# Optimization experiments

Measured on AMD Instinct MI355X. Metric: run time of the kernel, lower is better.

The kernel has to match this reference:

```python
import jax, jax.numpy as jnp
import numpy as np

N = 50000   # nodes
E = 800000  # edges
H = 128     # hidden_dim
H2 = H // 2


def setup_inputs() -> dict:
    key = jax.random.key(0)
    ks = jax.random.split(key, 12)
    s = 0.05  # weight scale for numerical sanity
    d = {}
    d['coord_x'] = jax.random.normal(ks[0], (N,), jnp.float32)
    d['coord_y'] = jax.random.normal(ks[1], (N,), jnp.float32)
    d['W1'] = jax.random.normal(ks[2], (3, H), jnp.float32) * s
    d['b1'] = jnp.zeros((H,), jnp.float32)
    d['W2'] = jax.random.normal(ks[3], (H, H), jnp.float32) * s
    d['b2'] = jnp.zeros((H,), jnp.float32)
    d['W3'] = jax.random.normal(ks[4], (H, H), jnp.float32) * s
    d['b3'] = jnp.zeros((H,), jnp.float32)
    d['W4'] = jax.random.normal(ks[5], (H, H), jnp.float32) * s
    d['b4'] = jnp.zeros((H,), jnp.float32)
    d['W5'] = jax.random.normal(ks[6], (H, H), jnp.float32) * s
    d['b5'] = jnp.zeros((H,), jnp.float32)
    d['Wl1'] = jax.random.normal(ks[7], (H, H2), jnp.float32) * s
    d['bl1'] = jnp.zeros((H2,), jnp.float32)
    d['Wl2'] = jax.random.normal(ks[8], (H2, 1), jnp.float32) * s
    d['bl2'] = jnp.zeros((1,), jnp.float32)
    d['src'] = jax.random.randint(ks[9], (E,), 0, N, dtype=jnp.int32)
    d['dst'] = jax.random.randint(ks[10], (E,), 0, N, dtype=jnp.int32)
    return d


def reference(coord_x, coord_y, W1, b1, W2, b2, W3, b3, W4, b4, W5, b5,
              Wl1, bl1, Wl2, bl2, src, dst):
    ones_e = jnp.ones((E,), jnp.float32)
    in_deg = jax.ops.segment_sum(ones_e, dst, num_segments=N)   # [N]
    out_deg = jax.ops.segment_sum(ones_e, src, num_segments=N)  # [N]
    # DGL GraphConv norm='both': D_out^{-1/2} on src side, D_in^{-1/2} on dst side,
    # degrees clamped to min 1.
    norm_s = (jnp.maximum(out_deg, 1.0) ** -0.5)[:, None]  # [N,1]
    norm_d = (jnp.maximum(in_deg, 1.0) ** -0.5)[:, None]   # [N,1]

    def gconv(h, W, b):
        msg = (h * norm_s)[src]                                   # [E,F] gather
        agg = jax.ops.segment_sum(msg, dst, num_segments=N)       # [N,F] scatter-add
        return (agg * norm_d) @ W + b

    # node features: [in_degree, x, y]
    h = jnp.stack([in_deg, coord_x, coord_y], axis=1)  # [N,3]
    for W, b in ((W1, b1), (W2, b2), (W3, b3), (W4, b4), (W5, b5)):
        h = jax.nn.relu(gconv(h, W, b))

    graph_emb = jnp.mean(h, axis=0, keepdims=True)          # [1,H] mean_nodes
    h_emb = jax.nn.relu(graph_emb @ Wl1 + bl1)              # dropout p=0 -> identity
    pred = jax.nn.sigmoid(h_emb @ Wl2 + bl2)                # [1,1]
    return pred, graph_emb, h
```

## Files before the change

### kernel.cpp

```cpp
#include <hip/hip_runtime.h>
#include <hip/hip_bf16.h>
#include <math.h>

#define NN 50000
#define NE 800000
#define HD 128
#define NB 196
#define CAP 5120
#define B1_EPB 1024

typedef __attribute__((ext_vector_type(8))) short bf16x8v;
typedef __attribute__((ext_vector_type(4))) float f32x4v;

static __device__ __forceinline__ unsigned short f2bf(float x) {
    union { float f; unsigned u; } v; v.f = x;
    unsigned r = v.u + 0x7fff + ((v.u >> 16) & 1);
    return (unsigned short)(r >> 16);
}

__global__ __launch_bounds__(256) void bucket_kernel(const int* __restrict__ src,
                                                     const int* __restrict__ dst,
                                                     int* __restrict__ dcur,
                                                     int* __restrict__ scur,
                                                     ushort2* __restrict__ dbucket,
                                                     unsigned short* __restrict__ sbucket) {
    __shared__ int hd[NB], hsb[NB], cd[NB], cs[NB];
    int t = threadIdx.x;
    if (t < NB) { hd[t] = 0; hsb[t] = 0; }
    __syncthreads();
    int d[4], s[4];
    int e0 = blockIdx.x * B1_EPB + t;
    #pragma unroll
    for (int j = 0; j < 4; ++j) {
        int e = e0 + j * 256;
        if (e < NE) {
            d[j] = dst[e]; s[j] = src[e];
            atomicAdd(&hd[d[j] >> 8], 1);
            atomicAdd(&hsb[s[j] >> 8], 1);
        } else d[j] = -1;
    }
    __syncthreads();
    if (t < NB) {
        cd[t] = atomicAdd(&dcur[t], hd[t]);
        cs[t] = atomicAdd(&scur[t], hsb[t]);
    }
    __syncthreads();
    #pragma unroll
    for (int j = 0; j < 4; ++j) {
        if (d[j] >= 0) {
            int b = d[j] >> 8;
            int p = atomicAdd(&cd[b], 1);
            if (p < CAP) dbucket[(long)b * CAP + p] = make_ushort2((unsigned short)d[j],
                                                                   (unsigned short)s[j]);
            int bs = s[j] >> 8;
            int p2 = atomicAdd(&cs[bs], 1);
            if (p2 < CAP) sbucket[(long)bs * CAP + p2] = (unsigned short)s[j];
        }
    }
}

__global__ __launch_bounds__(256) void csr_out_kernel(const ushort2* __restrict__ dbucket,
                                                      const int* __restrict__ dcur,
                                                      const unsigned short* __restrict__ sbucket,
                                                      const int* __restrict__ scur,
                                                      int* __restrict__ row_ptr,
                                                      unsigned short* __restrict__ col,
                                                      int* __restrict__ out_cnt) {
    __shared__ int buf[256];
    __shared__ int hist[256];
    __shared__ int cur[256];
    int k = blockIdx.x, t = threadIdx.x;

    int tot = (t < NB) ? min(dcur[t], CAP) : 0;
    buf[t] = tot;
    __syncthreads();
    for (int o = 1; o < 256; o <<= 1) {
        int a = (t >= o) ? buf[t - o] : 0;
        __syncthreads();
        buf[t] += a;
        __syncthreads();
    }
    int base = (k > 0) ? buf[k - 1] : 0;
    int cnt = min(dcur[k], CAP);

    hist[t] = 0;
    __syncthreads();
    const ushort2* bk = dbucket + (long)k * CAP;
    for (int e = t; e < cnt; e += 256) atomicAdd(&hist[bk[e].x & 255], 1);
    __syncthreads();
    int h = hist[t];

    buf[t] = h;
    __syncthreads();
    for (int o = 1; o < 256; o <<= 1) {
        int a = (t >= o) ? buf[t - o] : 0;
        __syncthreads();
        buf[t] += a;
        __syncthreads();
    }
    int start = base + buf[t] - h;
    int id = (k << 8) + t;
    if (id < NN) row_ptr[id] = start;
    if (k == NB - 1 && t == 0) row_ptr[NN] = base + cnt;
    cur[t] = start;
    __syncthreads();

    for (int e = t; e < cnt; e += 256) {
        ushort2 p = bk[e];
        int pos = atomicAdd(&cur[p.x & 255], 1);
        col[pos] = p.y;
    }

    __syncthreads();
    hist[t] = 0;
    __syncthreads();
    int scnt = min(scur[k], CAP);
    const unsigned short* sk = sbucket + (long)k * CAP;
    for (int e = t; e < scnt; e += 256) atomicAdd(&hist[sk[e] & 255], 1);
    __syncthreads();
    if (id < NN) out_cnt[id] = hist[t];
}

__global__ __launch_bounds__(256) void initw_kernel(const float* __restrict__ cx,
                                                    const float* __restrict__ cy,
                                                    const int* __restrict__ row_ptr,
                                                    const int* __restrict__ out_cnt,
                                                    const float* __restrict__ W2,
                                                    const float* __restrict__ W3,
                                                    const float* __restrict__ W4,
                                                    const float* __restrict__ W5,
                                                    float* __restrict__ norm_s,
                                                    float* __restrict__ norm_d,
                                                    float* __restrict__ h0s,
                                                    unsigned short* __restrict__ Wt,
                                                    float* __restrict__ embsum) {
    int bid = blockIdx.x, t = threadIdx.x;
    if (bid < NB) {
        int i = (bid << 8) + t;
        if (i < NN) {
            float id = (float)(row_ptr[i + 1] - row_ptr[i]);
            float od = (float)out_cnt[i];
            float ns = 1.0f / sqrtf(fmaxf(od, 1.0f));
            norm_s[i] = ns;
            norm_d[i] = 1.0f / sqrtf(fmaxf(id, 1.0f));
            h0s[i * 3 + 0] = id * ns;
            h0s[i * 3 + 1] = cx[i] * ns;
            h0s[i * 3 + 2] = cy[i] * ns;
        }
    } else {
        int gid = ((bid - NB) << 8) + t;
        int l = gid >> 14, idx = gid & 16383;
        int n = idx >> 7, k = idx & 127;
        const float* W = (l == 0) ? W2 : (l == 1) ? W3 : (l == 2) ? W4 : W5;
        Wt[gid] = f2bf(W[k * 128 + n]);
        if (bid == NB && t < 128) embsum[t] = 0.0f;
    }
}

__global__ __launch_bounds__(256) void layer1_kernel(const int* __restrict__ row_ptr,
                                                     const unsigned short* __restrict__ col,
                                                     const float* __restrict__ h0s,
                                                     const float* __restrict__ norm_d,
                                                     const float* __restrict__ norm_s,
                                                     const float* __restrict__ W1,
                                                     const float* __restrict__ b1,
                                                     unsigned short* __restrict__ h1s) {
    __shared__ float la3[256][3];
    __shared__ float lw[3][128];
    __shared__ float lb[128];
    int t = threadIdx.x;
    int n0 = blockIdx.x << 8;
    if (t < 128) {
        lw[0][t] = W1[t]; lw[1][t] = W1[128 + t]; lw[2][t] = W1[256 + t];
        lb[t] = b1[t];
    }
    int n = n0 + t;
    if (n < NN) {
        float a0 = 0.f, a1 = 0.f, a2 = 0.f;
        int end = row_ptr[n + 1];
        for (int e = row_ptr[n]; e < end; ++e) {
            int s = col[e];
            a0 += h0s[s * 3 + 0];
            a1 += h0s[s * 3 + 1];
            a2 += h0s[s * 3 + 2];
        }
        float nd = norm_d[n];
        la3[t][0] = a0 * nd; la3[t][1] = a1 * nd; la3[t][2] = a2 * nd;
    }
    __syncthreads();
    #pragma unroll 4
    for (int i = 0; i < 128; ++i) {
        int idx = (i << 8) + t;
        int r = idx >> 7, c = idx & 127;
        int nn = n0 + r;
        if (nn < NN) {
            float v = la3[r][0] * lw[0][c] + la3[r][1] * lw[1][c]
                    + la3[r][2] * lw[2][c] + lb[c];
            h1s[((long)nn << 7) + c] = f2bf(fmaxf(v, 0.f) * norm_s[nn]);
        }
    }
}

__global__ __launch_bounds__(256) void fused_layer16_kernel(const int* __restrict__ row_ptr,
                                                            const unsigned short* __restrict__ col,
                                                            const unsigned int* __restrict__ hin,
                                                            const float* __restrict__ norm_d,
                                                            const float* __restrict__ norm_s,
                                                            const unsigned short* __restrict__ Wt,
                                                            const float* __restrict__ bias,
                                                            unsigned short* __restrict__ hout,
                                                            float* __restrict__ out_f32,
                                                            float* __restrict__ embsum) {
    __shared__ unsigned int lA[16][68];
    __shared__ float ldscol[4][128];
    int t = threadIdx.x;
    int wv = t >> 6, lane = t & 63;
    int m0 = blockIdx.x << 4;

    const unsigned int* hb = hin + lane;
    #pragma unroll
    for (int half = 0; half < 2; ++half) {
        int rA = (half << 3) + wv;
        int rB = rA + 4;
        int nA = m0 + rA, nB = m0 + rB;
        int eA = row_ptr[nA], endA = row_ptr[nA + 1];
        int eB = row_ptr[nB], endB = row_ptr[nB + 1];
        float axA = 0.f, ayA = 0.f, axB = 0.f, ayB = 0.f;

        while (eA + 3 < endA && eB + 3 < endB) {
            unsigned uA[4], uB[4];
            #pragma unroll
            for (int j = 0; j < 4; ++j) uA[j] = hb[(long)col[eA + j] << 6];
            #pragma unroll
            for (int j = 0; j < 4; ++j) uB[j] = hb[(long)col[eB + j] << 6];
            #pragma unroll
            for (int j = 0; j < 4; ++j) {
                axA += __uint_as_float(uA[j] << 16);
                ayA += __uint_as_float(uA[j] & 0xffff0000u);
                axB += __uint_as_float(uB[j] << 16);
                ayB += __uint_as_float(uB[j] & 0xffff0000u);
            }
            eA += 4; eB += 4;
        }
        for (; eA + 3 < endA; eA += 4) {
            unsigned u[4];
            #pragma unroll
            for (int j = 0; j < 4; ++j) u[j] = hb[(long)col[eA + j] << 6];
            #pragma unroll
            for (int j = 0; j < 4; ++j) {
                axA += __uint_as_float(u[j] << 16);
                ayA += __uint_as_float(u[j] & 0xffff0000u);
            }
        }
        for (; eA < endA; ++eA) {
            unsigned u0 = hb[(long)col[eA] << 6];
            axA += __uint_as_float(u0 << 16);
            ayA += __uint_as_float(u0 & 0xffff0000u);
        }
        for (; eB + 3 < endB; eB += 4) {
            unsigned u[4];
            #pragma unroll
            for (int j = 0; j < 4; ++j) u[j] = hb[(long)col[eB + j] << 6];
            #pragma unroll
            for (int j = 0; j < 4; ++j) {
                axB += __uint_as_float(u[j] << 16);
                ayB += __uint_as_float(u[j] & 0xffff0000u);
            }
        }
        for (; eB < endB; ++eB) {
            unsigned u0 = hb[(long)col[eB] << 6];
            axB += __uint_as_float(u0 << 16);
            ayB += __uint_as_float(u0 & 0xffff0000u);
        }

        float ndA = norm_d[nA], ndB = norm_d[nB];
        lA[rA][lane] = (unsigned)f2bf(axA * ndA) | ((unsigned)f2bf(ayA * ndA) << 16);
        lA[rB][lane] = (unsigned)f2bf(axB * ndB) | ((unsigned)f2bf(ayB * ndB) << 16);
    }
    __syncthreads();

    int fr = lane & 15, kq = lane >> 4;
    bf16x8v a0 = *(const bf16x8v*)&lA[fr][ 0 + (kq << 2)];
    bf16x8v a1 = *(const bf16x8v*)&lA[fr][16 + (kq << 2)];
    bf16x8v a2 = *(const bf16x8v*)&lA[fr][32 + (kq << 2)];
    bf16x8v a3 = *(const bf16x8v*)&lA[fr][48 + (kq << 2)];

    float4 scv = make_float4(1.f, 1.f, 1.f, 1.f);
    if (!out_f32) scv = *(const float4*)(norm_s + m0 + (kq << 2));

    #pragma unroll
    for (int j = 0; j < 2; ++j) {
        int n0 = ((wv << 1) + j) << 4;
        const unsigned short* wb = Wt + ((n0 + fr) << 7) + (kq << 3);
        f32x4v acc = {0.f, 0.f, 0.f, 0.f};
        acc = __builtin_amdgcn_mfma_f32_16x16x32_bf16(a0, *(const bf16x8v*)(wb + 0),  acc, 0, 0, 0);
        acc = __builtin_amdgcn_mfma_f32_16x16x32_bf16(a1, *(const bf16x8v*)(wb + 32), acc, 0, 0, 0);
        acc = __builtin_amdgcn_mfma_f32_16x16x32_bf16(a2, *(const bf16x8v*)(wb + 64), acc, 0, 0, 0);
        acc = __builtin_amdgcn_mfma_f32_16x16x32_bf16(a3, *(const bf16x8v*)(wb + 96), acc, 0, 0, 0);

        int c = n0 + fr;
        float bv = bias[c];
        if (out_f32) {
            float cs = 0.f;
            #pragma unroll
            for (int r = 0; r < 4; ++r) {
                int mr = m0 + (kq << 2) + r;
                float v = fmaxf(acc[r] + bv, 0.f);
                out_f32[((long)mr << 7) + c] = v;
                cs += v;
            }
            ldscol[kq][c] = cs;
        } else {
            #pragma unroll
            for (int r = 0; r < 4; ++r) {
                int mr = m0 + (kq << 2) + r;
                float v = fmaxf(acc[r] + bv, 0.f);
                float sc = (r == 0) ? scv.x : (r == 1) ? scv.y : (r == 2) ? scv.z : scv.w;
                hout[((long)mr << 7) + c] = f2bf(v * sc);
            }
        }
    }

    if (out_f32) {
        __syncthreads();
        if (t < 128) {
            float s = ldscol[0][t] + ldscol[1][t] + ldscol[2][t] + ldscol[3][t];
            atomicAdd(&embsum[t], s);
        }
    }
}

__global__ __launch_bounds__(128) void head_kernel(const float* __restrict__ embsum,
                                                   const float* __restrict__ Wl1,
                                                   const float* __restrict__ bl1,
                                                   const float* __restrict__ Wl2,
                                                   const float* __restrict__ bl2,
                                                   float* __restrict__ d_out) {
    __shared__ float emb[128];
    __shared__ float hemb[64];
    int t = threadIdx.x;
    float e = embsum[t] * (1.0f / (float)NN);
    emb[t] = e;
    d_out[1 + t] = e;
    __syncthreads();
    if (t < 64) {
        float acc = bl1[t];
        for (int k = 0; k < 128; ++k)
            acc += emb[k] * Wl1[k * 64 + t];
        hemb[t] = fmaxf(acc, 0.f);
    }
    __syncthreads();
    if (t == 0) {
        float acc = bl2[0];
        for (int j = 0; j < 64; ++j)
            acc += hemb[j] * Wl2[j];
        d_out[0] = 1.0f / (1.0f + expf(-acc));
    }
}

extern "C" void kernel_launch(void* const* d_in, const int* in_sizes, int n_in,
                              void* d_out, int out_size, void* d_ws, size_t ws_size,
                              hipStream_t stream) {
    const float* cx  = (const float*)d_in[0];
    const float* cy  = (const float*)d_in[1];
    const float* W1  = (const float*)d_in[2];
    const float* b1  = (const float*)d_in[3];
    const float* W2  = (const float*)d_in[4];
    const float* b2  = (const float*)d_in[5];
    const float* W3  = (const float*)d_in[6];
    const float* b3  = (const float*)d_in[7];
    const float* W4  = (const float*)d_in[8];
    const float* b4  = (const float*)d_in[9];
    const float* W5  = (const float*)d_in[10];
    const float* b5  = (const float*)d_in[11];
    const float* Wl1 = (const float*)d_in[12];
    const float* bl1 = (const float*)d_in[13];
    const float* Wl2 = (const float*)d_in[14];
    const float* bl2 = (const float*)d_in[15];
    const int*   src = (const int*)d_in[16];
    const int*   dst = (const int*)d_in[17];

    float* out = (float*)d_out;
    float* h_out = out + 129;

    float* ws       = (float*)d_ws;
    float* norm_s   = ws;
    float* norm_d   = ws + NN;
    int*   out_cnt  = (int*)(ws + 2 * NN);
    int*   row_ptr  = (int*)(ws + 3 * NN);
    unsigned short* hsA = (unsigned short*)(ws + 4 * NN + 64);
    unsigned short* hsB = (unsigned short*)(ws + 68 * NN + 64);
    unsigned short* col = (unsigned short*)(ws + 132 * NN + 64);
    float* h0s      = ws + 148 * NN + 64;
    unsigned short* Wt = (unsigned short*)(ws + 154 * NN + 64);
    float* embsum   = ws + 154 * NN + 64 + 32768;
    int*   dcur     = (int*)(ws + 154 * NN + 33600);
    int*   scur     = dcur + NB;
    ushort2* dbucket = (ushort2*)(ws + 154 * NN + 34048);
    unsigned short* sbucket = (unsigned short*)(ws + 154 * NN + 34048 + NB * CAP);

    hipMemsetAsync(dcur, 0, 2 * NB * sizeof(int), stream);
    bucket_kernel<<<(NE + B1_EPB - 1) / B1_EPB, 256, 0, stream>>>(src, dst, dcur, scur,
                                                                  dbucket, sbucket);
    csr_out_kernel<<<NB, 256, 0, stream>>>(dbucket, dcur, sbucket, scur,
                                           row_ptr, col, out_cnt);

    initw_kernel<<<NB + 256, 256, 0, stream>>>(cx, cy, row_ptr, out_cnt,
                                               W2, W3, W4, W5,
                                               norm_s, norm_d, h0s, Wt, embsum);

    layer1_kernel<<<(NN + 255) / 256, 256, 0, stream>>>(row_ptr, col, h0s,
                                                        norm_d, norm_s, W1, b1, hsA);

    const float* bs[4] = {b2, b3, b4, b5};
    unsigned short* hcur = hsA;
    unsigned short* hnxt = hsB;
    for (int l = 0; l < 4; ++l) {
        bool last = (l == 3);
        fused_layer16_kernel<<<NN / 16, 256, 0, stream>>>(
            row_ptr, col, (const unsigned int*)hcur, norm_d, norm_s,
            Wt + l * 16384, bs[l],
            last ? nullptr : hnxt,
            last ? h_out : nullptr,
            last ? embsum : nullptr);
        unsigned short* tmp = hcur; hcur = hnxt; hnxt = tmp;
    }

    head_kernel<<<1, 128, 0, stream>>>(embsum, Wl1, bl1, Wl2, bl2, out);
}
```

Measured before the change: 329.7 us.

## Split last GCN layer into separate gather and MFMA GEMM kernels with sharded embsum

```diff
diff --git a/kernel.cpp b/kernel.cpp
--- a/kernel.cpp
+++ b/kernel.cpp
@@ -133,7 +133,7 @@
                                                     float* __restrict__ norm_d,
                                                     float* __restrict__ h0s,
                                                     unsigned short* __restrict__ Wt,
-                                                    float* __restrict__ embsum) {
+                                                    float* __restrict__ embsum8) {
     int bid = blockIdx.x, t = threadIdx.x;
     if (bid < NB) {
         int i = (bid << 8) + t;
@@ -153,7 +153,7 @@
         int n = idx >> 7, k = idx & 127;
         const float* W = (l == 0) ? W2 : (l == 1) ? W3 : (l == 2) ? W4 : W5;
         Wt[gid] = f2bf(W[k * 128 + n]);
-        if (bid == NB && t < 128) embsum[t] = 0.0f;
+        if (gid < 1024) embsum8[gid] = 0.0f;
     }
 }
 
@@ -208,11 +208,8 @@
                                                             const float* __restrict__ norm_s,
                                                             const unsigned short* __restrict__ Wt,
                                                             const float* __restrict__ bias,
-                                                            unsigned short* __restrict__ hout,
-                                                            float* __restrict__ out_f32,
-                                                            float* __restrict__ embsum) {
+                                                            unsigned short* __restrict__ hout) {
     __shared__ unsigned int lA[16][68];
-    __shared__ float ldscol[4][128];
     int t = threadIdx.x;
     int wv = t >> 6, lane = t & 63;
     int m0 = blockIdx.x << 4;
@@ -285,8 +282,7 @@
     bf16x8v a2 = *(const bf16x8v*)&lA[fr][32 + (kq << 2)];
     bf16x8v a3 = *(const bf16x8v*)&lA[fr][48 + (kq << 2)];
 
-    float4 scv = make_float4(1.f, 1.f, 1.f, 1.f);
-    if (!out_f32) scv = *(const float4*)(norm_s + m0 + (kq << 2));
+    float4 scv = *(const float4*)(norm_s + m0 + (kq << 2));
 
     #pragma unroll
     for (int j = 0; j < 2; ++j) {
@@ -300,37 +296,117 @@
 
         int c = n0 + fr;
         float bv = bias[c];
-        if (out_f32) {
-            float cs = 0.f;
-            #pragma unroll
-            for (int r = 0; r < 4; ++r) {
-                int mr = m0 + (kq << 2) + r;
+        #pragma unroll
+        for (int r = 0; r < 4; ++r) {
+            int mr = m0 + (kq << 2) + r;
+            float v = fmaxf(acc[r] + bv, 0.f);
+            float sc = (r == 0) ? scv.x : (r == 1) ? scv.y : (r == 2) ? scv.z : scv.w;
+            hout[((long)mr << 7) + c] = f2bf(v * sc);
+        }
+    }
+}
+
+__global__ __launch_bounds__(256) void gather_bf16_kernel(const int* __restrict__ row_ptr,
+                                                          const unsigned short* __restrict__ col,
+                                                          const unsigned int* __restrict__ hs2,
+                                                          const float* __restrict__ norm_d,
+                                                          unsigned int* __restrict__ aggb2) {
+    int t = threadIdx.x;
+    int wave = t >> 6;
+    int lane = t & 63;
+    int n = blockIdx.x * 4 + wave;
+    if (n >= NN) return;
+    int beg = row_ptr[n], end = row_ptr[n + 1];
+    float nd = norm_d[n];
+    const unsigned int* hb = hs2 + lane;
+    float ax = 0.f, ay = 0.f;
+    int e = beg;
+    for (; e + 7 < end; e += 8) {
+        unsigned u[8];
+        #pragma unroll
+        for (int j = 0; j < 8; ++j) u[j] = hb[(long)col[e + j] << 6];
+        #pragma unroll
+        for (int j = 0; j < 8; ++j) {
+            ax += __uint_as_float(u[j] << 16);
+            ay += __uint_as_float(u[j] & 0xffff0000u);
+        }
+    }
+    for (; e < end; ++e) {
+        unsigned u0 = hb[(long)col[e] << 6];
+        ax += __uint_as_float(u0 << 16);
+        ay += __uint_as_float(u0 & 0xffff0000u);
+    }
+    unsigned po = (unsigned)f2bf(ax * nd) | ((unsigned)f2bf(ay * nd) << 16);
+    aggb2[(n << 6) + lane] = po;
+}
+
+__global__ __launch_bounds__(256) void gemm_mfma_kernel(const unsigned short* __restrict__ aggb,
+                                                        const unsigned short* __restrict__ Wt,
+                                                        const float* __restrict__ bias,
+                                                        float* __restrict__ out_f32,
+                                                        float* __restrict__ embsum8) {
+    __shared__ unsigned short ldsw[128][136];
+    __shared__ float ldscol[4][4][128];
+
+    int t = threadIdx.x;
+    int wv = t >> 6, lane = t & 63;
+    int fr = lane & 15, kq = lane >> 4;
+    int m0 = blockIdx.x * 64 + wv * 16;
+
+    #pragma unroll
+    for (int i = 0; i < 8; ++i) {
+        int idx = t + 256 * i;
+        int r = idx >> 4;
+        int c8 = (idx & 15) << 3;
+        *(bf16x8v*)(&ldsw[r][c8]) = *(const bf16x8v*)(Wt + (r << 7) + c8);
+    }
+
+    int mrow = m0 + fr;
+    long abase = (long)((mrow < NN) ? mrow : 0) << 7;
+    bf16x8v a0 = *(const bf16x8v*)(aggb + abase + 0  + kq * 8);
+    bf16x8v a1 = *(const bf16x8v*)(aggb + abase + 32 + kq * 8);
+    bf16x8v a2 = *(const bf16x8v*)(aggb + abase + 64 + kq * 8);
+    bf16x8v a3 = *(const bf16x8v*)(aggb + abase + 96 + kq * 8);
+
+    __syncthreads();
+
+    #pragma unroll
+    for (int nt = 0; nt < 8; ++nt) {
+        int n0 = nt << 4;
+        f32x4v acc = {0.f, 0.f, 0.f, 0.f};
+        acc = __builtin_amdgcn_mfma_f32_16x16x32_bf16(a0, *(const bf16x8v*)(&ldsw[n0 + fr][0  + kq * 8]), acc, 0, 0, 0);
+        acc = __builtin_amdgcn_mfma_f32_16x16x32_bf16(a1, *(const bf16x8v*)(&ldsw[n0 + fr][32 + kq * 8]), acc, 0, 0, 0);
+        acc = __builtin_amdgcn_mfma_f32_16x16x32_bf16(a2, *(const bf16x8v*)(&ldsw[n0 + fr][64 + kq * 8]), acc, 0, 0, 0);
+        acc = __builtin_amdgcn_mfma_f32_16x16x32_bf16(a3, *(const bf16x8v*)(&ldsw[n0 + fr][96 + kq * 8]), acc, 0, 0, 0);
+
+        int c = n0 + fr;
+        float bv = bias[c];
+        float cs = 0.f;
+        #pragma unroll
+        for (int r = 0; r < 4; ++r) {
+            int mr = m0 + kq * 4 + r;
+            if (mr < NN) {
                 float v = fmaxf(acc[r] + bv, 0.f);
                 out_f32[((long)mr << 7) + c] = v;
                 cs += v;
             }
-            ldscol[kq][c] = cs;
-        } else {
-            #pragma unroll
-            for (int r = 0; r < 4; ++r) {
-                int mr = m0 + (kq << 2) + r;
-                float v = fmaxf(acc[r] + bv, 0.f);
-                float sc = (r == 0) ? scv.x : (r == 1) ? scv.y : (r == 2) ? scv.z : scv.w;
-                hout[((long)mr << 7) + c] = f2bf(v * sc);
-            }
-        }
-    }
-
-    if (out_f32) {
-        __syncthreads();
-        if (t < 128) {
-            float s = ldscol[0][t] + ldscol[1][t] + ldscol[2][t] + ldscol[3][t];
-            atomicAdd(&embsum[t], s);
-        }
-    }
-}
-
-__global__ __launch_bounds__(128) void head_kernel(const float* __restrict__ embsum,
+        }
+        ldscol[wv][kq][c] = cs;
+    }
+
+    __syncthreads();
+    if (t < 128) {
+        float s = 0.f;
+        #pragma unroll
+        for (int w = 0; w < 4; ++w)
+            #pragma unroll
+            for (int q = 0; q < 4; ++q)
+                s += ldscol[w][q][t];
+        atomicAdd(&embsum8[((blockIdx.x & 7) << 7) + t], s);
+    }
+}
+
+__global__ __launch_bounds__(128) void head_kernel(const float* __restrict__ embsum8,
                                                    const float* __restrict__ Wl1,
                                                    const float* __restrict__ bl1,
                                                    const float* __restrict__ Wl2,
@@ -339,7 +415,10 @@
     __shared__ float emb[128];
     __shared__ float hemb[64];
     int t = threadIdx.x;
-    float e = embsum[t] * (1.0f / (float)NN);
+    float e = 0.f;
+    #pragma unroll
+    for (int j = 0; j < 8; ++j) e += embsum8[(j << 7) + t];
+    e *= (1.0f / (float)NN);
     emb[t] = e;
     d_out[1 + t] = e;
     __syncthreads();
@@ -393,11 +472,11 @@
     unsigned short* col = (unsigned short*)(ws + 132 * NN + 64);
     float* h0s      = ws + 148 * NN + 64;
     unsigned short* Wt = (unsigned short*)(ws + 154 * NN + 64);
-    float* embsum   = ws + 154 * NN + 64 + 32768;
-    int*   dcur     = (int*)(ws + 154 * NN + 33600);
+    float* embsum8  = ws + 154 * NN + 64 + 32768;
+    int*   dcur     = (int*)(ws + 154 * NN + 34112);
     int*   scur     = dcur + NB;
-    ushort2* dbucket = (ushort2*)(ws + 154 * NN + 34048);
-    unsigned short* sbucket = (unsigned short*)(ws + 154 * NN + 34048 + NB * CAP);
+    ushort2* dbucket = (ushort2*)(ws + 154 * NN + 34560);
+    unsigned short* sbucket = (unsigned short*)(ws + 154 * NN + 34560 + NB * CAP);
 
     hipMemsetAsync(dcur, 0, 2 * NB * sizeof(int), stream);
     bucket_kernel<<<(NE + B1_EPB - 1) / B1_EPB, 256, 0, stream>>>(src, dst, dcur, scur,
@@ -407,24 +486,27 @@
 
     initw_kernel<<<NB + 256, 256, 0, stream>>>(cx, cy, row_ptr, out_cnt,
                                                W2, W3, W4, W5,
-                                               norm_s, norm_d, h0s, Wt, embsum);
+                                               norm_s, norm_d, h0s, Wt, embsum8);
 
     layer1_kernel<<<(NN + 255) / 256, 256, 0, stream>>>(row_ptr, col, h0s,
                                                         norm_d, norm_s, W1, b1, hsA);
 
-    const float* bs[4] = {b2, b3, b4, b5};
+    const float* bs[3] = {b2, b3, b4};
     unsigned short* hcur = hsA;
     unsigned short* hnxt = hsB;
-    for (int l = 0; l < 4; ++l) {
-        bool last = (l == 3);
+    for (int l = 0; l < 3; ++l) {
         fused_layer16_kernel<<<NN / 16, 256, 0, stream>>>(
             row_ptr, col, (const unsigned int*)hcur, norm_d, norm_s,
-            Wt + l * 16384, bs[l],
-            last ? nullptr : hnxt,
-            last ? h_out : nullptr,
-            last ? embsum : nullptr);
+            Wt + l * 16384, bs[l], hnxt);
         unsigned short* tmp = hcur; hcur = hnxt; hnxt = tmp;
     }
 
-    head_kernel<<<1, 128, 0, stream>>>(embsum, Wl1, bl1, Wl2, bl2, out);
-}
+    gather_bf16_kernel<<<(NN + 3) / 4, 256, 0, stream>>>(row_ptr, col,
+                                                         (const unsigned int*)hcur,
+                                                         norm_d,
+                                                         (unsigned int*)hnxt);
+    gemm_mfma_kernel<<<(NN + 63) / 64, 256, 0, stream>>>(hnxt, Wt + 3 * 16384, b5,
+                                                         h_out, embsum8);
+
+    head_kernel<<<1, 128, 0, stream>>>(embsum8, Wl1, bl1, Wl2, bl2, out);
+}
```

After: 287.6 us (median of 2 runs). -12.8%, faster.
